# Kernel optimization log

Measured on AMD Instinct MI355X. Metric: run time of the kernel, lower is better.

## Reference

```python
import jax, jax.numpy as jnp
import numpy as np

INPUT_DIM = 1024
EMBED_DIMS = 128


def setup_inputs() -> dict:
    key = jax.random.key(0)
    ks = jax.random.split(key, 7)
    s_in = 1.0 / np.sqrt(INPUT_DIM)
    x = jax.random.normal(ks[0], (4, 4096, INPUT_DIM), dtype=jnp.float32)
    Wq = jax.random.uniform(ks[1], (INPUT_DIM, EMBED_DIMS), jnp.float32, -s_in, s_in)
    bq = jax.random.uniform(ks[2], (EMBED_DIMS,), jnp.float32, -s_in, s_in)
    Wk = jax.random.uniform(ks[3], (INPUT_DIM, EMBED_DIMS), jnp.float32, -s_in, s_in)
    bk = jax.random.uniform(ks[4], (EMBED_DIMS,), jnp.float32, -s_in, s_in)
    Wv = jax.random.uniform(ks[5], (INPUT_DIM, EMBED_DIMS), jnp.float32, -s_in, s_in)
    bv = jax.random.uniform(ks[6], (EMBED_DIMS,), jnp.float32, -s_in, s_in)
    return {"x": x, "Wq": Wq, "bq": bq, "Wk": Wk, "bk": bk, "Wv": Wv, "bv": bv}


def reference(x, Wq, bq, Wk, bk, Wv, bv):
    # x: [B, L, C]
    Q = jnp.einsum('blc,cd->bld', x, Wq) + bq  # [B, L, D]
    K = jnp.einsum('blc,cd->bld', x, Wk) + bk
    V = jnp.einsum('blc,cd->bld', x, Wv) + bv
    d_k = Q.shape[-1]
    scores = jnp.einsum('bld,bmd->blm', Q, K) / jnp.sqrt(jnp.float32(d_k))  # [B, L, L]
    attn = jax.nn.softmax(scores, axis=-1)
    return jnp.einsum('blm,bmd->bld', attn, V)  # [B, L, D]
```

## Files before the change

### kernel.cpp

```cpp
#include <hip/hip_runtime.h>
#include <stdint.h>

typedef __bf16 bf16;
typedef __bf16 bf16x8 __attribute__((ext_vector_type(8)));
typedef __bf16 bf16x4 __attribute__((ext_vector_type(4)));
typedef _Float16 f16;
typedef f16 f16x8 __attribute__((ext_vector_type(8)));
typedef f16 f16x4 __attribute__((ext_vector_type(4)));
typedef f16 f16x2 __attribute__((ext_vector_type(2)));
typedef float f32x4 __attribute__((ext_vector_type(4)));
typedef float f32x16 __attribute__((ext_vector_type(16)));
typedef uint32_t u32x4 __attribute__((ext_vector_type(4)));

#define LQ    16384
#define CDIM  1024
#define DDIM  128
#define NSPLIT 4
#define QS 0.12751741f

static __device__ __forceinline__ uint32_t pkrtz(float a, float b) {
  return __builtin_bit_cast(uint32_t, __builtin_amdgcn_cvt_pkrtz(a, b));
}

__global__ void prep_kernel(const float* __restrict__ Wq, const float* __restrict__ Wk,
                            const float* __restrict__ Wv, const float* __restrict__ bq,
                            const float* __restrict__ bk, const float* __restrict__ bv,
                            bf16* __restrict__ Wt, float* __restrict__ bias_all) {
  int idx = blockIdx.x * 256 + threadIdx.x;
  int p = idx >> 17;
  int rem = idx & 131071;
  int k = rem >> 7, n = rem & 127;
  const float* W = (p == 0) ? Wq : (p == 1) ? Wk : Wv;
  float s = (p == 0) ? QS : 1.0f;
  Wt[(size_t)(p * 128 + n) * CDIM + k] = (bf16)(W[rem] * s);
  if (idx < 384) {
    int pp = idx >> 7, nn = idx & 127;
    const float* b = (pp == 0) ? bq : (pp == 1) ? bk : bv;
    bias_all[idx] = b[nn] * ((pp == 0) ? QS : 1.0f);
  }
}

__global__ __launch_bounds__(256, 2) void qkv_gemm(
    const float* __restrict__ x, const bf16* __restrict__ Wt,
    const float* __restrict__ bias_all,
    bf16* __restrict__ Qw, bf16* __restrict__ Kw, f16* __restrict__ Vtw) {
  __shared__ bf16 Al[2][128 * 72];
  __shared__ bf16 Bl[2][128 * 72];
  const int t = threadIdx.x;
  const int w = t >> 6;
  const int lane = t & 63;
  const int l15 = lane & 15;
  const int quad = lane >> 4;
  const int lin = blockIdx.y * 128 + blockIdx.x;
  const int logical = (lin & 7) * 48 + (lin >> 3);
  const int y = logical % 3;
  const int m0 = (logical / 3) * 128;
  const bf16* W = Wt + (size_t)y * (DDIM * CDIM);
  const int m_off = (w & 1) * 64;
  const int n_off = (w >> 1) * 64;

  f32x4 zero4 = {0.f, 0.f, 0.f, 0.f};
  f32x4 acc[4][4];
#pragma unroll
  for (int i = 0; i < 4; i++)
#pragma unroll
    for (int j = 0; j < 4; j++) acc[i][j] = zero4;

  const int xrr = t >> 4;
  const int xc = (t & 15) << 2;
  const int wr = t >> 3;
  const int wc = (t & 7) << 3;

  float4 xa[8];
  bf16x8 wa[4];
#pragma unroll
  for (int c = 0; c < 8; c++)
    xa[c] = *(const float4*)&x[(size_t)(m0 + c * 16 + xrr) * CDIM + xc];
#pragma unroll
  for (int c = 0; c < 4; c++)
    wa[c] = *(const bf16x8*)&W[(size_t)(c * 32 + wr) * CDIM + wc];

  for (int kc = 0; kc < 16; kc++) {
    bf16* Ab = Al[kc & 1];
    bf16* Bb = Bl[kc & 1];
#pragma unroll
    for (int c = 0; c < 8; c++) {
      bf16x4 v;
      v[0] = (bf16)xa[c].x; v[1] = (bf16)xa[c].y;
      v[2] = (bf16)xa[c].z; v[3] = (bf16)xa[c].w;
      *(bf16x4*)&Ab[(c * 16 + xrr) * 72 + xc] = v;
    }
#pragma unroll
    for (int c = 0; c < 4; c++)
      *(bf16x8*)&Bb[(c * 32 + wr) * 72 + wc] = wa[c];

    const int kn = (kc < 15 ? kc + 1 : 15) * 64;
#pragma unroll
    for (int c = 0; c < 8; c++)
      xa[c] = *(const float4*)&x[(size_t)(m0 + c * 16 + xrr) * CDIM + kn + xc];
#pragma unroll
    for (int c = 0; c < 4; c++)
      wa[c] = *(const bf16x8*)&W[(size_t)(c * 32 + wr) * CDIM + kn + wc];

    __syncthreads();

#pragma unroll
    for (int ks = 0; ks < 2; ks++) {
      bf16x8 af[4], bfr[4];
#pragma unroll
      for (int mt = 0; mt < 4; mt++)
        af[mt] = *(const bf16x8*)&Ab[(m_off + mt * 16 + l15) * 72 + ks * 32 + quad * 8];
#pragma unroll
      for (int nt = 0; nt < 4; nt++)
        bfr[nt] = *(const bf16x8*)&Bb[(n_off + nt * 16 + l15) * 72 + ks * 32 + quad * 8];
#pragma unroll
      for (int mt = 0; mt < 4; mt++)
#pragma unroll
        for (int nt = 0; nt < 4; nt++)
          acc[mt][nt] = __builtin_amdgcn_mfma_f32_16x16x32_bf16(af[mt], bfr[nt], acc[mt][nt], 0, 0, 0);
    }
  }

  float bias4[4];
#pragma unroll
  for (int nt = 0; nt < 4; nt++) bias4[nt] = bias_all[y * 128 + n_off + nt * 16 + l15];

  if (y < 2) {
    bf16* outp = (y == 0) ? Qw : Kw;
#pragma unroll
    for (int mt = 0; mt < 4; mt++)
#pragma unroll
      for (int nt = 0; nt < 4; nt++) {
        int n = n_off + nt * 16 + l15;
#pragma unroll
        for (int r = 0; r < 4; r++) {
          int m = m0 + m_off + mt * 16 + quad * 4 + r;
          outp[(size_t)m * DDIM + n] = (bf16)(acc[mt][nt][r] + bias4[nt]);
        }
      }
  } else {
#pragma unroll
    for (int mt = 0; mt < 4; mt++)
#pragma unroll
      for (int nt = 0; nt < 4; nt++) {
        int n = n_off + nt * 16 + l15;
        int m = m0 + m_off + mt * 16 + quad * 4;
        f16x4 pv;
#pragma unroll
        for (int r = 0; r < 4; r++) pv[r] = (f16)(acc[mt][nt][r] + bias4[nt]);
        *(f16x4*)&Vtw[(size_t)n * LQ + m] = pv;
      }
  }
}

__global__ __launch_bounds__(256, 2) void flash_kernel(
    const bf16* __restrict__ Qw, const bf16* __restrict__ Kw, const f16* __restrict__ Vtw,
    bf16* __restrict__ Opb, float* __restrict__ lp) {
  __shared__ bf16 Kl[2][64 * 136];
  __shared__ f16  Vl[2][128 * 72];

  const int t = threadIdx.x;
  const int w = t >> 6;
  const int lane = t & 63;
  const int l31 = lane & 31;
  const int hi = lane >> 5;
  const int lin = blockIdx.y * 128 + blockIdx.x;
  const int logical = ((lin & 7) << 6) + (lin >> 3);
  const int qb = logical & 127;
  const int sp = logical >> 7;
  const int batch = qb >> 5;
  const int q0w = qb * 128 + w * 32;
  const int kv_base = batch * 4096 + sp * 1024;

  bf16x8 qf[8];
#pragma unroll
  for (int ks = 0; ks < 8; ks++)
    qf[ks] = *(const bf16x8*)&Qw[(size_t)(q0w + l31) * DDIM + ks * 16 + hi * 8];

  const f32x16 z16 = {0.f,0.f,0.f,0.f,0.f,0.f,0.f,0.f,0.f,0.f,0.f,0.f,0.f,0.f,0.f,0.f};
  f32x16 o[4];
  o[0] = z16; o[1] = z16; o[2] = z16; o[3] = z16;
  f32x16 liacc = z16;

  f16x8 ones;
#pragma unroll
  for (int i = 0; i < 8; i++) ones[i] = (f16)1.f;

  const int kr = t >> 4;
  const int kcol = (t & 15) << 3;
  const int vr = t >> 3;
  const int vcol = (t & 7) << 3;

  bf16x8 ka[4];
  f16x8 va[4];
#pragma unroll
  for (int c = 0; c < 4; c++)
    ka[c] = *(const bf16x8*)&Kw[(size_t)(kv_base + c * 16 + kr) * DDIM + kcol];
#pragma unroll
  for (int c = 0; c < 4; c++)
    va[c] = *(const f16x8*)&Vtw[(size_t)(c * 32 + vr) * LQ + kv_base + vcol];

  for (int tile = 0; tile < 16; tile++) {
    bf16* Kb = Kl[tile & 1];
    f16*  Vb = Vl[tile & 1];
#pragma unroll
    for (int c = 0; c < 4; c++)
      *(bf16x8*)&Kb[(c * 16 + kr) * 136 + kcol] = ka[c];
#pragma unroll
    for (int c = 0; c < 4; c++)
      *(f16x8*)&Vb[(c * 32 + vr) * 72 + vcol] = va[c];

    const int kvn = kv_base + (tile < 15 ? tile + 1 : 15) * 64;
#pragma unroll
    for (int c = 0; c < 4; c++)
      ka[c] = *(const bf16x8*)&Kw[(size_t)(kvn + c * 16 + kr) * DDIM + kcol];
#pragma unroll
    for (int c = 0; c < 4; c++)
      va[c] = *(const f16x8*)&Vtw[(size_t)(c * 32 + vr) * LQ + kvn + vcol];

    __syncthreads();

    f32x16 sv0 = z16, sv1 = z16;
    __builtin_amdgcn_s_setprio(1);
#pragma unroll
    for (int ks = 0; ks < 8; ks++) {
      bf16x8 kf0 = *(const bf16x8*)&Kb[l31 * 136 + ks * 16 + hi * 8];
      bf16x8 kf1 = *(const bf16x8*)&Kb[(32 + l31) * 136 + ks * 16 + hi * 8];
      sv0 = __builtin_amdgcn_mfma_f32_32x32x16_bf16(kf0, qf[ks], sv0, 0, 0, 0);
      sv1 = __builtin_amdgcn_mfma_f32_32x32x16_bf16(kf1, qf[ks], sv1, 0, 0, 0);
    }
    __builtin_amdgcn_s_setprio(0);

#pragma unroll
    for (int r = 0; r < 16; r++) {
      sv0[r] = __builtin_amdgcn_exp2f(sv0[r]);
      sv1[r] = __builtin_amdgcn_exp2f(sv1[r]);
    }

#pragma unroll
    for (int mk = 0; mk < 2; mk++) {
      const f32x16 s = mk ? sv1 : sv0;
#pragma unroll
      for (int h = 0; h < 2; h++) {
        const int b = h * 8;
        uint32_t a0 = pkrtz(s[b + 0], s[b + 1]);
        uint32_t a1 = pkrtz(s[b + 2], s[b + 3]);
        uint32_t a2 = pkrtz(s[b + 4], s[b + 5]);
        uint32_t a3 = pkrtz(s[b + 6], s[b + 7]);
        asm("v_permlane32_swap_b32 %0, %1" : "+v"(a0), "+v"(a2));
        asm("v_permlane32_swap_b32 %0, %1" : "+v"(a1), "+v"(a3));
        u32x4 aw; aw.x = a0; aw.y = a1; aw.z = a2; aw.w = a3;
        f16x8 pa = __builtin_bit_cast(f16x8, aw);
        __builtin_amdgcn_s_setprio(1);
#pragma unroll
        for (int dt = 0; dt < 4; dt++) {
          f16x8 vf = *(const f16x8*)&Vb[(dt * 32 + l31) * 72 + mk * 32 + h * 16 + hi * 8];
          o[dt] = __builtin_amdgcn_mfma_f32_32x32x16_f16(pa, vf, o[dt], 0, 0, 0);
        }
        liacc = __builtin_amdgcn_mfma_f32_32x32x16_f16(pa, ones, liacc, 0, 0, 0);
        __builtin_amdgcn_s_setprio(0);
      }
    }
  }

  const size_t po = (size_t)sp * LQ * DDIM;
#pragma unroll
  for (int dt = 0; dt < 4; dt++)
#pragma unroll
    for (int r = 0; r < 16; r++) {
      int q = q0w + (r & 3) + 8 * (r >> 2) + 4 * hi;
      Opb[po + (size_t)q * DDIM + dt * 32 + l31] = (bf16)o[dt][r];
    }
  if (l31 == 0) {
#pragma unroll
    for (int r = 0; r < 16; r++)
      lp[(size_t)sp * LQ + q0w + (r & 3) + 8 * (r >> 2) + 4 * hi] = liacc[r];
  }
}

__global__ void combine_kernel(const bf16* __restrict__ Opb, const float* __restrict__ lp,
                               float* __restrict__ out) {
  int idx = blockIdx.x * 256 + threadIdx.x;
  int q = idx >> 5;
  int d = (idx & 31) * 4;
  float lsum = 0.f;
  float acc[4] = {0.f, 0.f, 0.f, 0.f};
#pragma unroll
  for (int sp = 0; sp < NSPLIT; sp++) {
    lsum += lp[(size_t)sp * LQ + q];
    bf16x4 ov = *(const bf16x4*)&Opb[(size_t)sp * LQ * DDIM + (size_t)q * DDIM + d];
#pragma unroll
    for (int j = 0; j < 4; j++) acc[j] += (float)ov[j];
  }
  float inv = 1.0f / lsum;
  float4 r;
  r.x = acc[0] * inv; r.y = acc[1] * inv; r.z = acc[2] * inv; r.w = acc[3] * inv;
  *(float4*)&out[(size_t)q * DDIM + d] = r;
}

extern "C" void kernel_launch(void* const* d_in, const int* in_sizes, int n_in,
                              void* d_out, int out_size, void* d_ws, size_t ws_size,
                              hipStream_t stream) {
  const float* x  = (const float*)d_in[0];
  const float* Wq = (const float*)d_in[1];
  const float* bq = (const float*)d_in[2];
  const float* Wk = (const float*)d_in[3];
  const float* bk = (const float*)d_in[4];
  const float* Wv = (const float*)d_in[5];
  const float* bv = (const float*)d_in[6];
  char* ws = (char*)d_ws;
  bf16* Qw   = (bf16*)(ws);
  bf16* Kw   = (bf16*)(ws + ((size_t)4 << 20));
  f16*  Vtw  = (f16*)(ws + ((size_t)8 << 20));
  bf16* Wt   = (bf16*)(ws + ((size_t)12 << 20));
  float* bias_all = (float*)(ws + ((size_t)12 << 20) + 786432);
  bf16* Opb  = (bf16*)(ws + ((size_t)13 << 20));
  float* lpp = (float*)(ws + ((size_t)29 << 20));
  float* out = (float*)d_out;

  prep_kernel<<<1536, 256, 0, stream>>>(Wq, Wk, Wv, bq, bk, bv, Wt, bias_all);
  qkv_gemm<<<dim3(128, 3), 256, 0, stream>>>(x, Wt, bias_all, Qw, Kw, Vtw);
  flash_kernel<<<dim3(128, NSPLIT), 256, 0, stream>>>(Qw, Kw, Vtw, Opb, lpp);
  combine_kernel<<<2048, 256, 0, stream>>>(Opb, lpp, out);
}
```

Before: 180.7 us.

## Retile QKV GEMM to 128x64 tiles with 32x32 MFMA and XOR-swizzled LDS

The QKV projection GEMM moves from 128x128 output tiles (384 blocks) to 128x64 tiles (768 blocks) and from 16x16x32 to 32x32x16 bf16 MFMA. Padded shared-memory rows are replaced by an XOR swizzle, and the launch bound goes to 3 blocks per CU. The aim is more blocks across the 256 CUs, higher occupancy and fewer LDS reads per MFMA. In exchange, each x tile is now loaded and converted twice as often (once per 64-column half), which raises global traffic on the fp32 input.

```diff
diff --git a/kernel.cpp b/kernel.cpp
--- a/kernel.cpp
+++ b/kernel.cpp
@@ -40,115 +40,112 @@
   }
 }
 
-__global__ __launch_bounds__(256, 2) void qkv_gemm(
+__global__ __launch_bounds__(256, 3) void qkv_gemm(
     const float* __restrict__ x, const bf16* __restrict__ Wt,
     const float* __restrict__ bias_all,
     bf16* __restrict__ Qw, bf16* __restrict__ Kw, f16* __restrict__ Vtw) {
-  __shared__ bf16 Al[2][128 * 72];
-  __shared__ bf16 Bl[2][128 * 72];
+  __shared__ bf16 As[2][128 * 64];
+  __shared__ bf16 Bs[2][64 * 64];
   const int t = threadIdx.x;
   const int w = t >> 6;
   const int lane = t & 63;
-  const int l15 = lane & 15;
-  const int quad = lane >> 4;
-  const int lin = blockIdx.y * 128 + blockIdx.x;
-  const int logical = (lin & 7) * 48 + (lin >> 3);
-  const int y = logical % 3;
-  const int m0 = (logical / 3) * 128;
-  const bf16* W = Wt + (size_t)y * (DDIM * CDIM);
+  const int l31 = lane & 31;
+  const int hi = lane >> 5;
+  const int lin = blockIdx.x;
+  const int logical = (lin & 7) * 96 + (lin >> 3);
+  const int mi = logical / 6;
+  const int rr = logical % 6;
+  const int y = rr >> 1;
+  const int nb = rr & 1;
+  const int m0 = mi * 128;
+  const int n0 = nb * 64;
+  const bf16* W = Wt + (size_t)y * (DDIM * CDIM) + (size_t)n0 * CDIM;
   const int m_off = (w & 1) * 64;
-  const int n_off = (w >> 1) * 64;
-
-  f32x4 zero4 = {0.f, 0.f, 0.f, 0.f};
-  f32x4 acc[4][4];
-#pragma unroll
-  for (int i = 0; i < 4; i++)
-#pragma unroll
-    for (int j = 0; j < 4; j++) acc[i][j] = zero4;
-
-  const int xrr = t >> 4;
-  const int xc = (t & 15) << 2;
-  const int wr = t >> 3;
-  const int wc = (t & 7) << 3;
-
-  float4 xa[8];
-  bf16x8 wa[4];
-#pragma unroll
-  for (int c = 0; c < 8; c++)
-    xa[c] = *(const float4*)&x[(size_t)(m0 + c * 16 + xrr) * CDIM + xc];
-#pragma unroll
-  for (int c = 0; c < 4; c++)
-    wa[c] = *(const bf16x8*)&W[(size_t)(c * 32 + wr) * CDIM + wc];
+  const int n_off = (w >> 1) * 32;
+
+  const f32x16 z16 = {0.f,0.f,0.f,0.f,0.f,0.f,0.f,0.f,0.f,0.f,0.f,0.f,0.f,0.f,0.f,0.f};
+  f32x16 acc[2];
+  acc[0] = z16; acc[1] = z16;
+
+  const int srow = t >> 3;
+  const int g = t & 7;
+  const int sg = (g ^ (srow & 7)) * 8;
+  const int scol = g * 8;
+
+  float4 xa[4][2];
+  bf16x8 wa[2];
+#pragma unroll
+  for (int c = 0; c < 4; c++) {
+    const float* p = &x[(size_t)(m0 + c * 32 + srow) * CDIM + scol];
+    xa[c][0] = *(const float4*)p;
+    xa[c][1] = *(const float4*)(p + 4);
+  }
+#pragma unroll
+  for (int c = 0; c < 2; c++)
+    wa[c] = *(const bf16x8*)&W[(size_t)(c * 32 + srow) * CDIM + scol];
 
   for (int kc = 0; kc < 16; kc++) {
-    bf16* Ab = Al[kc & 1];
-    bf16* Bb = Bl[kc & 1];
-#pragma unroll
-    for (int c = 0; c < 8; c++) {
-      bf16x4 v;
-      v[0] = (bf16)xa[c].x; v[1] = (bf16)xa[c].y;
-      v[2] = (bf16)xa[c].z; v[3] = (bf16)xa[c].w;
-      *(bf16x4*)&Ab[(c * 16 + xrr) * 72 + xc] = v;
-    }
-#pragma unroll
-    for (int c = 0; c < 4; c++)
-      *(bf16x8*)&Bb[(c * 32 + wr) * 72 + wc] = wa[c];
+    bf16* Ab = As[kc & 1];
+    bf16* Bb = Bs[kc & 1];
+#pragma unroll
+    for (int c = 0; c < 4; c++) {
+      bf16x8 v;
+      v[0] = (bf16)xa[c][0].x; v[1] = (bf16)xa[c][0].y;
+      v[2] = (bf16)xa[c][0].z; v[3] = (bf16)xa[c][0].w;
+      v[4] = (bf16)xa[c][1].x; v[5] = (bf16)xa[c][1].y;
+      v[6] = (bf16)xa[c][1].z; v[7] = (bf16)xa[c][1].w;
+      *(bf16x8*)&Ab[(c * 32 + srow) * 64 + sg] = v;
+    }
+#pragma unroll
+    for (int c = 0; c < 2; c++)
+      *(bf16x8*)&Bb[(c * 32 + srow) * 64 + sg] = wa[c];
 
     const int kn = (kc < 15 ? kc + 1 : 15) * 64;
 #pragma unroll
-    for (int c = 0; c < 8; c++)
-      xa[c] = *(const float4*)&x[(size_t)(m0 + c * 16 + xrr) * CDIM + kn + xc];
-#pragma unroll
-    for (int c = 0; c < 4; c++)
-      wa[c] = *(const bf16x8*)&W[(size_t)(c * 32 + wr) * CDIM + kn + wc];
+    for (int c = 0; c < 4; c++) {
+      const float* p = &x[(size_t)(m0 + c * 32 + srow) * CDIM + kn + scol];
+      xa[c][0] = *(const float4*)p;
+      xa[c][1] = *(const float4*)(p + 4);
+    }
+#pragma unroll
+    for (int c = 0; c < 2; c++)
+      wa[c] = *(const bf16x8*)&W[(size_t)(c * 32 + srow) * CDIM + kn + scol];
 
     __syncthreads();
 
 #pragma unroll
-    for (int ks = 0; ks < 2; ks++) {
-      bf16x8 af[4], bfr[4];
-#pragma unroll
-      for (int mt = 0; mt < 4; mt++)
-        af[mt] = *(const bf16x8*)&Ab[(m_off + mt * 16 + l15) * 72 + ks * 32 + quad * 8];
-#pragma unroll
-      for (int nt = 0; nt < 4; nt++)
-        bfr[nt] = *(const bf16x8*)&Bb[(n_off + nt * 16 + l15) * 72 + ks * 32 + quad * 8];
-#pragma unroll
-      for (int mt = 0; mt < 4; mt++)
-#pragma unroll
-        for (int nt = 0; nt < 4; nt++)
-          acc[mt][nt] = __builtin_amdgcn_mfma_f32_16x16x32_bf16(af[mt], bfr[nt], acc[mt][nt], 0, 0, 0);
-    }
-  }
-
-  float bias4[4];
-#pragma unroll
-  for (int nt = 0; nt < 4; nt++) bias4[nt] = bias_all[y * 128 + n_off + nt * 16 + l15];
+    for (int ks = 0; ks < 4; ks++) {
+      const int rg = ((ks * 2 + hi) ^ (l31 & 7)) * 8;
+      bf16x8 bfr = *(const bf16x8*)&Bb[(n_off + l31) * 64 + rg];
+      bf16x8 af0 = *(const bf16x8*)&Ab[(m_off + l31) * 64 + rg];
+      bf16x8 af1 = *(const bf16x8*)&Ab[(m_off + 32 + l31) * 64 + rg];
+      acc[0] = __builtin_amdgcn_mfma_f32_32x32x16_bf16(af0, bfr, acc[0], 0, 0, 0);
+      acc[1] = __builtin_amdgcn_mfma_f32_32x32x16_bf16(af1, bfr, acc[1], 0, 0, 0);
+    }
+  }
+
+  const float bias = bias_all[y * 128 + n0 + n_off + l31];
+  const int n = n0 + n_off + l31;
 
   if (y < 2) {
     bf16* outp = (y == 0) ? Qw : Kw;
 #pragma unroll
-    for (int mt = 0; mt < 4; mt++)
-#pragma unroll
-      for (int nt = 0; nt < 4; nt++) {
-        int n = n_off + nt * 16 + l15;
-#pragma unroll
-        for (int r = 0; r < 4; r++) {
-          int m = m0 + m_off + mt * 16 + quad * 4 + r;
-          outp[(size_t)m * DDIM + n] = (bf16)(acc[mt][nt][r] + bias4[nt]);
-        }
+    for (int mt = 0; mt < 2; mt++)
+#pragma unroll
+      for (int r = 0; r < 16; r++) {
+        int m = m0 + m_off + mt * 32 + (r & 3) + 8 * (r >> 2) + 4 * hi;
+        outp[(size_t)m * DDIM + n] = (bf16)(acc[mt][r] + bias);
       }
   } else {
 #pragma unroll
-    for (int mt = 0; mt < 4; mt++)
-#pragma unroll
-      for (int nt = 0; nt < 4; nt++) {
-        int n = n_off + nt * 16 + l15;
-        int m = m0 + m_off + mt * 16 + quad * 4;
+    for (int mt = 0; mt < 2; mt++)
+#pragma unroll
+      for (int gq = 0; gq < 4; gq++) {
+        int mbase = m0 + m_off + mt * 32 + 8 * gq + 4 * hi;
         f16x4 pv;
 #pragma unroll
-        for (int r = 0; r < 4; r++) pv[r] = (f16)(acc[mt][nt][r] + bias4[nt]);
-        *(f16x4*)&Vtw[(size_t)n * LQ + m] = pv;
+        for (int r = 0; r < 4; r++) pv[r] = (f16)(acc[mt][gq * 4 + r] + bias);
+        *(f16x4*)&Vtw[(size_t)n * LQ + mbase] = pv;
       }
   }
 }
@@ -319,7 +316,7 @@
   float* out = (float*)d_out;
 
   prep_kernel<<<1536, 256, 0, stream>>>(Wq, Wk, Wv, bq, bk, bv, Wt, bias_all);
-  qkv_gemm<<<dim3(128, 3), 256, 0, stream>>>(x, Wt, bias_all, Qw, Kw, Vtw);
+  qkv_gemm<<<768, 256, 0, stream>>>(x, Wt, bias_all, Qw, Kw, Vtw);
   flash_kernel<<<dim3(128, NSPLIT), 256, 0, stream>>>(Qw, Kw, Vtw, Opb, lpp);
   combine_kernel<<<2048, 256, 0, stream>>>(Opb, lpp, out);
 }
```

Result: slower. 184.7 us (+2.2%).
